# Optimization experiments

Hardware: AMD Instinct MI355X
Metric: run time of the kernel (lower is better)

Reference implementation:

```python
import jax, jax.numpy as jnp
import numpy as np

BATCH = 4096
IN_CAPS = 64
OUT_CAPS = 16
IN_DIM = 64
OUT_DIM = 64
NUM_ITER = 3
LN_EPS = 1e-5


def setup_inputs() -> dict:
    key = jax.random.key(0)
    ks = jax.random.split(key, 13)
    n = lambda k, s: jax.random.normal(k, s, dtype=jnp.float32)
    return {
        "x_inp": n(ks[0], (BATCH, IN_CAPS, IN_DIM)),
        "W_A": n(ks[1], (IN_CAPS, IN_DIM)),
        "B_A": n(ks[2], (IN_CAPS,)),
        "W_F1": n(ks[3], (IN_CAPS, IN_DIM, IN_DIM)),
        "W_F2": n(ks[4], (OUT_CAPS, IN_DIM, OUT_DIM)),
        "B_F2": n(ks[5], (OUT_CAPS, OUT_DIM)),
        "W_G1": n(ks[6], (OUT_DIM, OUT_DIM)),
        "W_G2": n(ks[7], (OUT_CAPS, OUT_DIM, IN_DIM)),
        "B_G2": n(ks[8], (OUT_CAPS, IN_DIM)),
        "ln_gamma": jnp.ones((OUT_DIM,), jnp.float32),
        "ln_beta": jnp.zeros((OUT_DIM,), jnp.float32),
        "W_S": n(ks[9], (IN_CAPS, OUT_CAPS, IN_DIM)),
        "B_S": n(ks[10], (IN_CAPS, OUT_CAPS)),
        "beta_use": n(ks[11], (IN_CAPS, OUT_CAPS)),
        "beta_ign": n(ks[12], (IN_CAPS, OUT_CAPS)),
    }


def _layer_norm(x, gamma, beta):
    mu = jnp.mean(x, axis=-1, keepdims=True)
    var = jnp.var(x, axis=-1, keepdims=True)  # biased, matches torch LayerNorm
    return (x - mu) * jax.lax.rsqrt(var + LN_EPS) * gamma + beta


def reference(x_inp, W_A, B_A, W_F1, W_F2, B_F2, W_G1, W_G2, B_G2,
              ln_gamma, ln_beta, W_S, B_S, beta_use, beta_ign):
    B = x_inp.shape[0]
    inv_sqrt = np.float32(1.0 / np.sqrt(IN_DIM))
    # activation logits per input capsule: [B, in_caps]
    a_e = jnp.einsum('bif,if->bi', x_inp, W_A) * inv_sqrt + B_A
    f_a_e = jax.nn.sigmoid(a_e)  # loop-invariant
    # temp_F is loop-invariant: [B, in_caps, in_dim]
    temp_F = jnp.einsum('bif,ifh->bih', x_inp, W_F1) * inv_sqrt
    R_em = jnp.full((B, IN_CAPS, OUT_CAPS), 1.0 / OUT_CAPS, dtype=x_inp.dtype)
    x_out = None
    for _ in range(NUM_ITER):
        D_use = f_a_e[:, :, None] * R_em                      # [B,i,m]
        D_ign = f_a_e[:, :, None] - D_use                     # [B,i,m]
        phi_em = beta_use * D_use - beta_ign * D_ign          # [B,i,m]
        temp_F_routed = phi_em.sum(axis=-1)[:, :, None] * temp_F  # [B,i,h]
        x_out = jnp.einsum('bih,mhd->bmd', temp_F_routed, W_F2) + B_F2  # [B,m,d]
        x_out_norm = _layer_norm(x_out, ln_gamma, ln_beta)
        temp_G = jnp.einsum('bmd,dh->bmh', x_out_norm, W_G1)  # [B,m,d]
        x_inp_hat = jnp.einsum('bmh,mhi->bmi', temp_G, W_G2) + B_G2  # [B,m,f]
        consistency = jnp.einsum('bif,bmf,imf->bim', x_inp, x_inp_hat, W_S) + B_S
        R_em = jax.nn.softmax(consistency, axis=-1)  # exp(log_softmax)
    return x_out
```

## Files before the change

### kernel.cpp

```cpp
#include <hip/hip_runtime.h>
#include <math.h>

#define IC 64
#define OC 16
#define DIM 64

typedef __attribute__((ext_vector_type(8))) short bf16x8;
typedef __attribute__((ext_vector_type(4))) float f32x4;

__device__ __forceinline__ unsigned short f2bf(float f) {
    unsigned int b = __float_as_uint(f);
    b += 0x7fffu + ((b >> 16) & 1u);
    return (unsigned short)(b >> 16);
}
__device__ __forceinline__ float bf2f(unsigned short h) {
    return __uint_as_float(((unsigned int)h) << 16);
}

__global__ void kSetup(const float* __restrict__ W_F2, const float* __restrict__ W_S,
                       const float* __restrict__ B_S, const float* __restrict__ bu,
                       const float* __restrict__ bi_, const float* __restrict__ W_G1,
                       const float* __restrict__ W_G2,
                       float* __restrict__ WSt2,
                       unsigned short* __restrict__ W1h, unsigned short* __restrict__ W1l,
                       unsigned short* __restrict__ W2h, unsigned short* __restrict__ W2l,
                       float* __restrict__ BSt, float* __restrict__ cb,
                       float* __restrict__ db, float* __restrict__ eb)
{
    int e = blockIdx.x * 256 + threadIdx.x;
    {
        int h = e >> 10, m = (e >> 6) & 15, d = e & 63;
        float v = W_F2[((size_t)m * 64 + h) * 64 + d];
        unsigned short hh = f2bf(v);
        size_t o = ((size_t)m * 64 + d) * 64 + h;
        W1h[o] = hh; W1l[o] = f2bf(v - bf2f(hh));
    }
    {
        int m = e >> 12, fo = (e >> 8) & 15, i = (e >> 2) & 63, fi = e & 3;
        WSt2[e] = W_S[((size_t)i * 16 + m) * 64 + fo * 4 + fi];
    }
    {
        int m = e >> 12, d = (e >> 6) & 63, f = e & 63;
        const float* g1 = W_G1 + d * 64;
        const float* g2 = W_G2 + (size_t)m * 4096 + f;
        float a = 0.f;
#pragma unroll 8
        for (int h = 0; h < 64; h++) a += g1[h] * g2[h * 64];
        unsigned short hh = f2bf(a);
        size_t o = ((size_t)m * 64 + f) * 64 + d;
        W2h[o] = hh; W2l[o] = f2bf(a - bf2f(hh));
    }
    if (e < 1024) {
        int m = e >> 6, i = e & 63;
        BSt[e] = B_S[i * 16 + m];
        cb[e] = bu[e] + bi_[e];
    }
    if (e < 64) {
        float sc = 0.f, sd = 0.f;
        for (int m = 0; m < 16; m++) {
            sc += bu[e * 16 + m] + bi_[e * 16 + m];
            sd += bi_[e * 16 + m];
        }
        db[e] = sd;
        eb[e] = sc * (1.0f / 16.0f) - sd;
    }
}

__global__ __launch_bounds__(256, 4)
void kT(const float* __restrict__ x, const float* __restrict__ W_A,
        const float* __restrict__ B_A, const float* __restrict__ eb,
        float* __restrict__ xq, float* __restrict__ fa, float* __restrict__ phi)
{
    __shared__ float Xs[2 * 64 * 65];
    const int t = threadIdx.x;
    const int blk = blockIdx.x;

    const float4* x4 = (const float4*)x;
#pragma unroll
    for (int s = 0; s < 8; s++) {
        int p = s * 256 + t;
        float4 v = x4[(size_t)blk * 2048 + p];
        int b = p >> 10, i = (p >> 4) & 63, fo = p & 15;
        float* row = &Xs[(b * 64 + i) * 65 + fo * 4];
        row[0] = v.x; row[1] = v.y; row[2] = v.z; row[3] = v.w;
    }
    __syncthreads();

    const int lane = t & 63, w = t >> 6;
#pragma unroll
    for (int s = 0; s < 8; s++) {
        int idx = s * 4 + w;
        int b = idx >> 4, fo = idx & 15;
        const float* row = &Xs[(b * 64 + lane) * 65 + fo * 4];
        ((float4*)xq)[((size_t)(blk * 2 + b) * 16 + fo) * 64 + lane] =
            make_float4(row[0], row[1], row[2], row[3]);
    }

    {
        int p = t >> 1, h = t & 1;
        int b = p >> 6, i = p & 63;
        const float* row = &Xs[(b * 64 + i) * 65 + h * 32];
        const float* wa = W_A + i * 64 + h * 32;
        float v = 0.f;
#pragma unroll
        for (int j = 0; j < 32; j++) v += row[j] * wa[j];
        v += __shfl_xor(v, 1);
        if (h == 0) {
            float ae = v * 0.125f + B_A[i];
            float fv = 1.0f / (1.0f + expf(-ae));
            size_t o = (size_t)(blk * 2 + b) * 64 + i;
            fa[o] = fv;
            phi[o] = fv * eb[i];
        }
    }
}

__global__ __launch_bounds__(256, 4)
void kA(const float* __restrict__ x, const float* __restrict__ W_F1,
        float* __restrict__ tF)
{
    __shared__ unsigned short Ah[64][72], Al[64][72];
    __shared__ unsigned short Bh[64][72], Bl[64][72];
    const int i = blockIdx.y;
    const int b0 = blockIdx.x * 64;
    const int t = threadIdx.x;
    const int bl = t >> 2, q = t & 3;

    {
        const float* src = x + ((size_t)(b0 + bl) * IC + i) * DIM + q * 4;
#pragma unroll
        for (int j4 = 0; j4 < 4; j4++) {
            float4 v = *(const float4*)(src + j4 * 16);
            int f = q * 4 + j4 * 16;
            float vv[4] = {v.x, v.y, v.z, v.w};
            ushort4 h4, l4;
            unsigned short hh;
            hh = f2bf(vv[0]); h4.x = hh; l4.x = f2bf(vv[0] - bf2f(hh));
            hh = f2bf(vv[1]); h4.y = hh; l4.y = f2bf(vv[1] - bf2f(hh));
            hh = f2bf(vv[2]); h4.z = hh; l4.z = f2bf(vv[2] - bf2f(hh));
            hh = f2bf(vv[3]); h4.w = hh; l4.w = f2bf(vv[3] - bf2f(hh));
            *(ushort4*)&Ah[bl][f] = h4;
            *(ushort4*)&Al[bl][f] = l4;
        }
        const float* wsrc = W_F1 + ((size_t)i * DIM + bl) * DIM + q * 4;
#pragma unroll
        for (int j4 = 0; j4 < 4; j4++) {
            float4 v = *(const float4*)(wsrc + j4 * 16);
            int h0 = q * 4 + j4 * 16;
            float vv[4] = {v.x, v.y, v.z, v.w};
#pragma unroll
            for (int c = 0; c < 4; c++) {
                unsigned short hh = f2bf(vv[c]);
                Bh[h0 + c][bl] = hh;
                Bl[h0 + c][bl] = f2bf(vv[c] - bf2f(hh));
            }
        }
    }
    __syncthreads();

    const int w = t >> 6, lane = t & 63;
    const int fm = lane & 15, fq = lane >> 4;
    const int r0 = w * 16;
    f32x4 acc[4];
#pragma unroll
    for (int nt = 0; nt < 4; nt++) {
        acc[nt][0] = 0.f; acc[nt][1] = 0.f; acc[nt][2] = 0.f; acc[nt][3] = 0.f;
    }

#pragma unroll
    for (int ks = 0; ks < 2; ks++) {
        const int kk = ks * 32 + fq * 8;
        bf16x8 ah = *(const bf16x8*)&Ah[r0 + fm][kk];
        bf16x8 al = *(const bf16x8*)&Al[r0 + fm][kk];
#pragma unroll
        for (int nt = 0; nt < 4; nt++) {
            bf16x8 bh = *(const bf16x8*)&Bh[nt * 16 + fm][kk];
            bf16x8 bl2 = *(const bf16x8*)&Bl[nt * 16 + fm][kk];
            acc[nt] = __builtin_amdgcn_mfma_f32_16x16x32_bf16(ah, bh, acc[nt], 0, 0, 0);
            acc[nt] = __builtin_amdgcn_mfma_f32_16x16x32_bf16(ah, bl2, acc[nt], 0, 0, 0);
            acc[nt] = __builtin_amdgcn_mfma_f32_16x16x32_bf16(al, bh, acc[nt], 0, 0, 0);
        }
    }

#pragma unroll
    for (int nt = 0; nt < 4; nt++)
#pragma unroll
        for (int j = 0; j < 4; j++) {
            int row = r0 + fq * 4 + j;
            int col = nt * 16 + fm;
            tF[((size_t)(b0 + row) * IC + i) * DIM + col] = acc[nt][j] * 0.125f;
        }
}

__global__ __launch_bounds__(256, 4)
void kS(const float* __restrict__ phi, const float* __restrict__ tF,
        float* __restrict__ s)
{
    __shared__ float ph[4 * 64];
    const int t = threadIdx.x;
    const int b0 = blockIdx.x * 4;
    ph[t] = phi[(size_t)b0 * 64 + t];
    __syncthreads();

    const int w = t >> 6, lane = t & 63;
    const int ig = lane >> 4, hq = lane & 15;
    const int b = b0 + w;
    const float4* tf4 = (const float4*)(tF + ((size_t)b * 64 + ig * 16) * 64) + hq;
    float4 a = make_float4(0.f, 0.f, 0.f, 0.f);
#pragma unroll
    for (int k = 0; k < 16; k++) {
        float p = ph[w * 64 + ig * 16 + k];
        float4 v = tf4[k * 16];
        a.x += p * v.x; a.y += p * v.y; a.z += p * v.z; a.w += p * v.w;
    }
#pragma unroll
    for (int k = 16; k <= 32; k <<= 1) {
        a.x += __shfl_xor(a.x, k); a.y += __shfl_xor(a.y, k);
        a.z += __shfl_xor(a.z, k); a.w += __shfl_xor(a.w, k);
    }
    if (ig == 0)
        ((float4*)(s + (size_t)b * 64))[hq] = a;
}

__global__ __launch_bounds__(256, 4)
void kXG(const float* __restrict__ s,
         const unsigned short* __restrict__ W1h, const unsigned short* __restrict__ W1l,
         const float* __restrict__ B_F2,
         const unsigned short* __restrict__ W2h, const unsigned short* __restrict__ W2l,
         const float* __restrict__ B_G2,
         const float* __restrict__ gam, const float* __restrict__ bet,
         float* __restrict__ xhat, float* __restrict__ out, const int last)
{
    __shared__ unsigned short Ah[64][72], Al[64][72];
    __shared__ unsigned short Bh[64][72], Bl[64][72];
    const int b0 = blockIdx.x * 64;
    const int m = blockIdx.y;
    const int t = threadIdx.x;
    const int bl = t >> 2, q = t & 3;

    {
        const float* src = s + (size_t)(b0 + bl) * DIM + q * 16;
#pragma unroll
        for (int j4 = 0; j4 < 4; j4++) {
            float4 v = ((const float4*)src)[j4];
            int f = q * 16 + j4 * 4;
            float vv[4] = {v.x, v.y, v.z, v.w};
            ushort4 h4, l4;
            unsigned short hh;
            hh = f2bf(vv[0]); h4.x = hh; l4.x = f2bf(vv[0] - bf2f(hh));
            hh = f2bf(vv[1]); h4.y = hh; l4.y = f2bf(vv[1] - bf2f(hh));
            hh = f2bf(vv[2]); h4.z = hh; l4.z = f2bf(vv[2] - bf2f(hh));
            hh = f2bf(vv[3]); h4.w = hh; l4.w = f2bf(vv[3] - bf2f(hh));
            *(ushort4*)&Ah[bl][f] = h4;
            *(ushort4*)&Al[bl][f] = l4;
        }
        const size_t wo = ((size_t)m * 64 + bl) * 64 + q * 16;
#pragma unroll
        for (int part = 0; part < 2; part++) {
            *(uint4*)&Bh[bl][q * 16 + part * 8] = *(const uint4*)(W1h + wo + part * 8);
            *(uint4*)&Bl[bl][q * 16 + part * 8] = *(const uint4*)(W1l + wo + part * 8);
        }
    }
    __syncthreads();

    const int w = t >> 6, lane = t & 63;
    const int fm = lane & 15, fq = lane >> 4;
    const int r0 = w * 16;
    f32x4 acc[4];
#pragma unroll
    for (int nt = 0; nt < 4; nt++) {
        acc[nt][0] = 0.f; acc[nt][1] = 0.f; acc[nt][2] = 0.f; acc[nt][3] = 0.f;
    }
#pragma unroll
    for (int ks = 0; ks < 2; ks++) {
        const int kk = ks * 32 + fq * 8;
        bf16x8 ah = *(const bf16x8*)&Ah[r0 + fm][kk];
        bf16x8 al = *(const bf16x8*)&Al[r0 + fm][kk];
#pragma unroll
        for (int nt = 0; nt < 4; nt++) {
            bf16x8 bh = *(const bf16x8*)&Bh[nt * 16 + fm][kk];
            bf16x8 bl2 = *(const bf16x8*)&Bl[nt * 16 + fm][kk];
            acc[nt] = __builtin_amdgcn_mfma_f32_16x16x32_bf16(ah, bh, acc[nt], 0, 0, 0);
            acc[nt] = __builtin_amdgcn_mfma_f32_16x16x32_bf16(ah, bl2, acc[nt], 0, 0, 0);
            acc[nt] = __builtin_amdgcn_mfma_f32_16x16x32_bf16(al, bh, acc[nt], 0, 0, 0);
        }
    }
#pragma unroll
    for (int nt = 0; nt < 4; nt++) {
        float bf = B_F2[m * DIM + nt * 16 + fm];
#pragma unroll
        for (int j = 0; j < 4; j++) acc[nt][j] += bf;
    }

    if (last) {
#pragma unroll
        for (int nt = 0; nt < 4; nt++)
#pragma unroll
            for (int j = 0; j < 4; j++) {
                int row = r0 + fq * 4 + j;
                out[((size_t)(b0 + row) * OC + m) * DIM + nt * 16 + fm] = acc[nt][j];
            }
        return;
    }

    {
        float g4[4], b4[4];
#pragma unroll
        for (int nt = 0; nt < 4; nt++) {
            g4[nt] = gam[nt * 16 + fm];
            b4[nt] = bet[nt * 16 + fm];
        }
#pragma unroll
        for (int j = 0; j < 4; j++) {
            float sum = acc[0][j] + acc[1][j] + acc[2][j] + acc[3][j];
            float sq = acc[0][j] * acc[0][j] + acc[1][j] * acc[1][j] +
                       acc[2][j] * acc[2][j] + acc[3][j] * acc[3][j];
#pragma unroll
            for (int k = 1; k <= 8; k <<= 1) {
                sum += __shfl_xor(sum, k);
                sq  += __shfl_xor(sq, k);
            }
            float mu = sum * (1.0f / 64.0f);
            float var = sq * (1.0f / 64.0f) - mu * mu;
            float rs = 1.0f / sqrtf(var + 1e-5f);
#pragma unroll
            for (int nt = 0; nt < 4; nt++)
                acc[nt][j] = (acc[nt][j] - mu) * rs * g4[nt] + b4[nt];
        }
    }
    __syncthreads();

    {
#pragma unroll
        for (int nt = 0; nt < 4; nt++)
#pragma unroll
            for (int j = 0; j < 4; j++) {
                float v = acc[nt][j];
                unsigned short hh = f2bf(v);
                int row = r0 + fq * 4 + j, col = nt * 16 + fm;
                Ah[row][col] = hh;
                Al[row][col] = f2bf(v - bf2f(hh));
            }
        const size_t wo = ((size_t)m * 64 + bl) * 64 + q * 16;
#pragma unroll
        for (int part = 0; part < 2; part++) {
            *(uint4*)&Bh[bl][q * 16 + part * 8] = *(const uint4*)(W2h + wo + part * 8);
            *(uint4*)&Bl[bl][q * 16 + part * 8] = *(const uint4*)(W2l + wo + part * 8);
        }
    }
    __syncthreads();

    f32x4 xh[4];
#pragma unroll
    for (int nt = 0; nt < 4; nt++) {
        float bg = B_G2[m * DIM + nt * 16 + fm];
        xh[nt][0] = bg; xh[nt][1] = bg; xh[nt][2] = bg; xh[nt][3] = bg;
    }
#pragma unroll
    for (int ks = 0; ks < 2; ks++) {
        const int kk = ks * 32 + fq * 8;
        bf16x8 ah = *(const bf16x8*)&Ah[r0 + fm][kk];
        bf16x8 al = *(const bf16x8*)&Al[r0 + fm][kk];
#pragma unroll
        for (int nt = 0; nt < 4; nt++) {
            bf16x8 bh = *(const bf16x8*)&Bh[nt * 16 + fm][kk];
            bf16x8 bl2 = *(const bf16x8*)&Bl[nt * 16 + fm][kk];
            xh[nt] = __builtin_amdgcn_mfma_f32_16x16x32_bf16(ah, bh, xh[nt], 0, 0, 0);
            xh[nt] = __builtin_amdgcn_mfma_f32_16x16x32_bf16(ah, bl2, xh[nt], 0, 0, 0);
            xh[nt] = __builtin_amdgcn_mfma_f32_16x16x32_bf16(al, bh, xh[nt], 0, 0, 0);
        }
    }
#pragma unroll
    for (int nt = 0; nt < 4; nt++)
#pragma unroll
        for (int j = 0; j < 4; j++) {
            int row = r0 + fq * 4 + j;
            xhat[((size_t)(b0 + row) * OC + m) * DIM + nt * 16 + fm] = xh[nt][j];
        }
}

__global__ __launch_bounds__(256, 4)
void kC(const float* __restrict__ xq, const float* __restrict__ xhat,
        const float* __restrict__ WSt2, const float* __restrict__ BSt,
        const float* __restrict__ cb, const float* __restrict__ db,
        const float* __restrict__ fa, const float* __restrict__ tF,
        float* __restrict__ s)
{
    __shared__ float buf[4 * 64 * 17];
    __shared__ float phs[4][64];
    const int b0 = blockIdx.x * 4;
    const int t = threadIdx.x;
    const int w = t >> 6, lane = t & 63;

    {
        const float4* src = (const float4*)(xhat + (size_t)b0 * OC * DIM);
        float4* dst = (float4*)buf;
#pragma unroll
        for (int j = 0; j < 4; j++) dst[t + j * 256] = src[t + j * 256];
    }
    __syncthreads();

    float acc[4][4];
#pragma unroll
    for (int k = 0; k < 4; k++) {
        float bs = BSt[(w * 4 + k) * IC + lane];
#pragma unroll
        for (int g = 0; g < 4; g++) acc[g][k] = bs;
    }

    const float4* xq4 = (const float4*)xq;
    for (int fc = 0; fc < 64; fc += 8) {
        const int fo = fc >> 2;
        float wreg[4][8];
#pragma unroll
        for (int k = 0; k < 4; k++) {
            int m = w * 4 + k;
#pragma unroll
            for (int q2 = 0; q2 < 2; q2++) {
                float4 v = *(const float4*)&WSt2[(((size_t)m * 16 + fo + q2) * IC + lane) * 4];
                wreg[k][q2 * 4 + 0] = v.x; wreg[k][q2 * 4 + 1] = v.y;
                wreg[k][q2 * 4 + 2] = v.z; wreg[k][q2 * 4 + 3] = v.w;
            }
        }
#pragma unroll
        for (int g = 0; g < 4; g++) {
            float xr[8];
#pragma unroll
            for (int q2 = 0; q2 < 2; q2++) {
                float4 v = xq4[((size_t)(b0 + g) * 16 + fo + q2) * 64 + lane];
                xr[q2 * 4 + 0] = v.x; xr[q2 * 4 + 1] = v.y;
                xr[q2 * 4 + 2] = v.z; xr[q2 * 4 + 3] = v.w;
            }
#pragma unroll
            for (int k = 0; k < 4; k++) {
                int m = w * 4 + k;
                const float* hp = &buf[(g * OC + m) * DIM + fc];
                float hr[8];
#pragma unroll
                for (int q2 = 0; q2 < 2; q2++) {
                    float4 v = *(const float4*)(hp + q2 * 4);
                    hr[q2 * 4 + 0] = v.x; hr[q2 * 4 + 1] = v.y;
                    hr[q2 * 4 + 2] = v.z; hr[q2 * 4 + 3] = v.w;
                }
#pragma unroll
                for (int ff = 0; ff < 8; ff++)
                    acc[g][k] += xr[ff] * hr[ff] * wreg[k][ff];
            }
        }
    }
    __syncthreads();
#pragma unroll
    for (int g = 0; g < 4; g++)
#pragma unroll
        for (int k = 0; k < 4; k++)
            buf[(g * IC + lane) * 17 + w * 4 + k] = acc[g][k];
    __syncthreads();

    {
        int g = t >> 6, i = t & 63;
        const float* row = &buf[(g * IC + i) * 17];
        float v[16], mx = -1e30f;
#pragma unroll
        for (int m = 0; m < OC; m++) { v[m] = row[m]; mx = fmaxf(mx, v[m]); }
        float sum = 0.f;
#pragma unroll
        for (int m = 0; m < OC; m++) { v[m] = expf(v[m] - mx); sum += v[m]; }
        float inv = 1.0f / sum;
        float a2 = 0.f;
#pragma unroll
        for (int m = 0; m < OC; m++) a2 += v[m] * inv * cb[i * OC + m];
        phs[g][i] = fa[(size_t)(b0 + g) * IC + i] * (a2 - db[i]);
    }
    __syncthreads();

    {
        const int ig = lane >> 4, hq = lane & 15;
        const int b = b0 + w;
        const float4* tf4 = (const float4*)(tF + ((size_t)b * 64 + ig * 16) * 64) + hq;
        float4 a = make_float4(0.f, 0.f, 0.f, 0.f);
#pragma unroll
        for (int k = 0; k < 16; k++) {
            float p = phs[w][ig * 16 + k];
            float4 v = tf4[k * 16];
            a.x += p * v.x; a.y += p * v.y; a.z += p * v.z; a.w += p * v.w;
        }
#pragma unroll
        for (int k = 16; k <= 32; k <<= 1) {
            a.x += __shfl_xor(a.x, k); a.y += __shfl_xor(a.y, k);
            a.z += __shfl_xor(a.z, k); a.w += __shfl_xor(a.w, k);
        }
        if (ig == 0)
            ((float4*)(s + (size_t)b * 64))[hq] = a;
    }
}

extern "C" void kernel_launch(void* const* d_in, const int* in_sizes, int n_in,
                              void* d_out, int out_size, void* d_ws, size_t ws_size,
                              hipStream_t stream)
{
    const float* x    = (const float*)d_in[0];
    const float* W_A  = (const float*)d_in[1];
    const float* B_A  = (const float*)d_in[2];
    const float* W_F1 = (const float*)d_in[3];
    const float* W_F2 = (const float*)d_in[4];
    const float* B_F2 = (const float*)d_in[5];
    const float* W_G1 = (const float*)d_in[6];
    const float* W_G2 = (const float*)d_in[7];
    const float* B_G2 = (const float*)d_in[8];
    const float* gam  = (const float*)d_in[9];
    const float* bet  = (const float*)d_in[10];
    const float* W_S  = (const float*)d_in[11];
    const float* B_S  = (const float*)d_in[12];
    const float* bu   = (const float*)d_in[13];
    const float* bi_  = (const float*)d_in[14];

    float* ws   = (float*)d_ws;
    float* tF   = ws;
    float* xq   = tF + 16777216;
    float* fa   = xq + 16777216;
    float* phi  = fa + 262144;
    float* s    = phi + 262144;
    float* xhat = s + 262144;
    float* WSt2 = xhat + 4194304;
    unsigned short* W1h = (unsigned short*)(WSt2 + 65536);
    unsigned short* W1l = W1h + 65536;
    unsigned short* W2h = W1l + 65536;
    unsigned short* W2l = W2h + 65536;
    float* BSt  = (float*)(W2l + 65536);
    float* cb   = BSt + 1024;
    float* db   = cb + 1024;
    float* eb   = db + 64;
    float* out  = (float*)d_out;

    kSetup<<<256, 256, 0, stream>>>(W_F2, W_S, B_S, bu, bi_, W_G1, W_G2,
                                    WSt2, W1h, W1l, W2h, W2l, BSt, cb, db, eb);
    kT<<<2048, 256, 0, stream>>>(x, W_A, B_A, eb, xq, fa, phi);
    kA<<<dim3(64, 64), 256, 0, stream>>>(x, W_F1, tF);
    kS<<<1024, 256, 0, stream>>>(phi, tF, s);
    for (int it = 0; it < 3; ++it) {
        kXG<<<dim3(64, 16), 256, 0, stream>>>(s, W1h, W1l, B_F2, W2h, W2l, B_G2,
                                              gam, bet, xhat, out, it == 2 ? 1 : 0);
        if (it < 2)
            kC<<<1024, 256, 0, stream>>>(xq, xhat, WSt2, BSt, cb, db, fa, tF, s);
    }
}
```

Measured before the change: 285.5 us.

## Double batch per kC block and read xhat through uniform scalar loads

kC now handles 8 batch rows per 512-thread block, not 4 per 256-thread block. Each wave pair splits across batch halves while sharing the same W_S slice. The shared-memory staging of xhat and its barrier are removed. Each wave instead reads xhat with wave-uniform addresses marked via readfirstlane, so the loads can go through the scalar path. This is meant to cut LDS traffic and a sync point, but it relies on scalar-cache bandwidth and larger blocks, which may lower occupancy.

Measured after the change: 312.1 us. 1.09x slower.

```diff
diff --git a/kernel.cpp b/kernel.cpp
--- a/kernel.cpp
+++ b/kernel.cpp
@@ -379,42 +379,35 @@
         }
 }
 
-__global__ __launch_bounds__(256, 4)
+__global__ __launch_bounds__(512, 4)
 void kC(const float* __restrict__ xq, const float* __restrict__ xhat,
         const float* __restrict__ WSt2, const float* __restrict__ BSt,
         const float* __restrict__ cb, const float* __restrict__ db,
         const float* __restrict__ fa, const float* __restrict__ tF,
         float* __restrict__ s)
 {
-    __shared__ float buf[4 * 64 * 17];
-    __shared__ float phs[4][64];
-    const int b0 = blockIdx.x * 4;
+    __shared__ float buf[8 * 64 * 17];
+    __shared__ float phs[8][64];
+    const int b0 = blockIdx.x * 8;
     const int t = threadIdx.x;
     const int w = t >> 6, lane = t & 63;
-
-    {
-        const float4* src = (const float4*)(xhat + (size_t)b0 * OC * DIM);
-        float4* dst = (float4*)buf;
-#pragma unroll
-        for (int j = 0; j < 4; j++) dst[t + j * 256] = src[t + j * 256];
-    }
-    __syncthreads();
+    const int mq = w & 3, gh = w >> 2;
 
     float acc[4][4];
 #pragma unroll
     for (int k = 0; k < 4; k++) {
-        float bs = BSt[(w * 4 + k) * IC + lane];
-#pragma unroll
-        for (int g = 0; g < 4; g++) acc[g][k] = bs;
+        float bs = BSt[(mq * 4 + k) * IC + lane];
+#pragma unroll
+        for (int gg = 0; gg < 4; gg++) acc[gg][k] = bs;
     }
 
     const float4* xq4 = (const float4*)xq;
-    for (int fc = 0; fc < 64; fc += 8) {
-        const int fo = fc >> 2;
+    for (int fo8 = 0; fo8 < 8; fo8++) {
+        const int fo = fo8 * 2, fc = fo8 * 8;
         float wreg[4][8];
 #pragma unroll
         for (int k = 0; k < 4; k++) {
-            int m = w * 4 + k;
+            int m = mq * 4 + k;
 #pragma unroll
             for (int q2 = 0; q2 < 2; q2++) {
                 float4 v = *(const float4*)&WSt2[(((size_t)m * 16 + fo + q2) * IC + lane) * 4];
@@ -423,7 +416,8 @@
             }
         }
 #pragma unroll
-        for (int g = 0; g < 4; g++) {
+        for (int gg = 0; gg < 4; gg++) {
+            int g = gh * 4 + gg;
             float xr[8];
 #pragma unroll
             for (int q2 = 0; q2 < 2; q2++) {
@@ -433,27 +427,23 @@
             }
 #pragma unroll
             for (int k = 0; k < 4; k++) {
-                int m = w * 4 + k;
-                const float* hp = &buf[(g * OC + m) * DIM + fc];
-                float hr[8];
-#pragma unroll
-                for (int q2 = 0; q2 < 2; q2++) {
-                    float4 v = *(const float4*)(hp + q2 * 4);
-                    hr[q2 * 4 + 0] = v.x; hr[q2 * 4 + 1] = v.y;
-                    hr[q2 * 4 + 2] = v.z; hr[q2 * 4 + 3] = v.w;
-                }
+                int m = mq * 4 + k;
+                int uo = __builtin_amdgcn_readfirstlane(
+                    (int)(((b0 + g) * 16 + m) * 64 + fc));
+                float4 h0 = *(const float4*)(xhat + uo);
+                float4 h1 = *(const float4*)(xhat + uo + 4);
+                float hs[8] = {h0.x, h0.y, h0.z, h0.w, h1.x, h1.y, h1.z, h1.w};
 #pragma unroll
                 for (int ff = 0; ff < 8; ff++)
-                    acc[g][k] += xr[ff] * hr[ff] * wreg[k][ff];
-            }
-        }
-    }
-    __syncthreads();
-#pragma unroll
-    for (int g = 0; g < 4; g++)
+                    acc[gg][k] += (xr[ff] * wreg[k][ff]) * hs[ff];
+            }
+        }
+    }
+#pragma unroll
+    for (int gg = 0; gg < 4; gg++)
 #pragma unroll
         for (int k = 0; k < 4; k++)
-            buf[(g * IC + lane) * 17 + w * 4 + k] = acc[g][k];
+            buf[((gh * 4 + gg) * IC + lane) * 17 + mq * 4 + k] = acc[gg][k];
     __syncthreads();
 
     {
@@ -541,6 +531,6 @@
         kXG<<<dim3(64, 16), 256, 0, stream>>>(s, W1h, W1l, B_F2, W2h, W2l, B_G2,
                                               gam, bet, xhat, out, it == 2 ? 1 : 0);
         if (it < 2)
-            kC<<<1024, 256, 0, stream>>>(xq, xhat, WSt2, BSt, cb, db, fa, tF, s);
-    }
-}
+            kC<<<512, 512, 0, stream>>>(xq, xhat, WSt2, BSt, cb, db, fa, tF, s);
+    }
+}
```

## Merge setup and transpose kernels; precompute split-bf16 transposed W_F1

Applied to the files above, without the earlier changes.

The weight-setup kernel and the x-transpose/activation kernel are merged into one launch, with the first 256 blocks doing setup and the rest doing the transpose. The eb term is now recomputed per input capsule inside the transpose path, so that path no longer depends on setup output. W_F1 is converted once into transposed bf16 hi/lo arrays, and kA loads these with vector copies instead of converting and scattering W_F1 in every one of its 4096 blocks. This removes one launch and the redundant per-block conversion, at the cost of extra workspace and a small redundant loop over the beta parameters.

New measurement: 279.3 us. 2.2% less time.

```diff
diff --git a/kernel.cpp b/kernel.cpp
--- a/kernel.cpp
+++ b/kernel.cpp
@@ -17,63 +17,71 @@
     return __uint_as_float(((unsigned int)h) << 16);
 }
 
-__global__ void kSetup(const float* __restrict__ W_F2, const float* __restrict__ W_S,
-                       const float* __restrict__ B_S, const float* __restrict__ bu,
-                       const float* __restrict__ bi_, const float* __restrict__ W_G1,
-                       const float* __restrict__ W_G2,
-                       float* __restrict__ WSt2,
-                       unsigned short* __restrict__ W1h, unsigned short* __restrict__ W1l,
-                       unsigned short* __restrict__ W2h, unsigned short* __restrict__ W2l,
-                       float* __restrict__ BSt, float* __restrict__ cb,
-                       float* __restrict__ db, float* __restrict__ eb)
+__global__ __launch_bounds__(256, 4)
+void kF1(const float* __restrict__ W_F2, const float* __restrict__ W_S,
+         const float* __restrict__ B_S, const float* __restrict__ bu,
+         const float* __restrict__ bi_, const float* __restrict__ W_G1,
+         const float* __restrict__ W_G2, const float* __restrict__ W_F1,
+         const float* __restrict__ x, const float* __restrict__ W_A,
+         const float* __restrict__ B_A,
+         float* __restrict__ WSt2,
+         unsigned short* __restrict__ W1h, unsigned short* __restrict__ W1l,
+         unsigned short* __restrict__ W2h, unsigned short* __restrict__ W2l,
+         unsigned short* __restrict__ WF1Th, unsigned short* __restrict__ WF1Tl,
+         float* __restrict__ BSt, float* __restrict__ cb, float* __restrict__ db,
+         float* __restrict__ xq, float* __restrict__ fa, float* __restrict__ phi)
 {
-    int e = blockIdx.x * 256 + threadIdx.x;
-    {
-        int h = e >> 10, m = (e >> 6) & 15, d = e & 63;
-        float v = W_F2[((size_t)m * 64 + h) * 64 + d];
-        unsigned short hh = f2bf(v);
-        size_t o = ((size_t)m * 64 + d) * 64 + h;
-        W1h[o] = hh; W1l[o] = f2bf(v - bf2f(hh));
-    }
-    {
-        int m = e >> 12, fo = (e >> 8) & 15, i = (e >> 2) & 63, fi = e & 3;
-        WSt2[e] = W_S[((size_t)i * 16 + m) * 64 + fo * 4 + fi];
-    }
-    {
-        int m = e >> 12, d = (e >> 6) & 63, f = e & 63;
-        const float* g1 = W_G1 + d * 64;
-        const float* g2 = W_G2 + (size_t)m * 4096 + f;
-        float a = 0.f;
+    if (blockIdx.x < 256) {
+        int e = blockIdx.x * 256 + threadIdx.x;
+        {
+            int h = e >> 10, m = (e >> 6) & 15, d = e & 63;
+            float v = W_F2[((size_t)m * 64 + h) * 64 + d];
+            unsigned short hh = f2bf(v);
+            size_t o = ((size_t)m * 64 + d) * 64 + h;
+            W1h[o] = hh; W1l[o] = f2bf(v - bf2f(hh));
+        }
+        {
+            int m = e >> 12, fo = (e >> 8) & 15, i = (e >> 2) & 63, fi = e & 3;
+            WSt2[e] = W_S[((size_t)i * 16 + m) * 64 + fo * 4 + fi];
+        }
+        {
+            int m = e >> 12, d = (e >> 6) & 63, f = e & 63;
+            const float* g1 = W_G1 + d * 64;
+            const float* g2 = W_G2 + (size_t)m * 4096 + f;
+            float a = 0.f;
 #pragma unroll 8
-        for (int h = 0; h < 64; h++) a += g1[h] * g2[h * 64];
-        unsigned short hh = f2bf(a);
-        size_t o = ((size_t)m * 64 + f) * 64 + d;
-        W2h[o] = hh; W2l[o] = f2bf(a - bf2f(hh));
-    }
-    if (e < 1024) {
-        int m = e >> 6, i = e & 63;
-        BSt[e] = B_S[i * 16 + m];
-        cb[e] = bu[e] + bi_[e];
-    }
-    if (e < 64) {
-        float sc = 0.f, sd = 0.f;
-        for (int m = 0; m < 16; m++) {
-            sc += bu[e * 16 + m] + bi_[e * 16 + m];
-            sd += bi_[e * 16 + m];
-        }
-        db[e] = sd;
-        eb[e] = sc * (1.0f / 16.0f) - sd;
-    }
-}
-
-__global__ __launch_bounds__(256, 4)
-void kT(const float* __restrict__ x, const float* __restrict__ W_A,
-        const float* __restrict__ B_A, const float* __restrict__ eb,
-        float* __restrict__ xq, float* __restrict__ fa, float* __restrict__ phi)
-{
+            for (int h = 0; h < 64; h++) a += g1[h] * g2[h * 64];
+            unsigned short hh = f2bf(a);
+            size_t o = ((size_t)m * 64 + f) * 64 + d;
+            W2h[o] = hh; W2l[o] = f2bf(a - bf2f(hh));
+        }
+        {
+#pragma unroll
+            for (int r = 0; r < 4; r++) {
+                int idx = r * 65536 + e;
+                int i = idx >> 12, h = (idx >> 6) & 63, f = idx & 63;
+                float v = W_F1[(((size_t)i * 64 + f) * 64) + h];
+                unsigned short hh = f2bf(v);
+                size_t o = ((size_t)i * 64 + h) * 64 + f;
+                WF1Th[o] = hh; WF1Tl[o] = f2bf(v - bf2f(hh));
+            }
+        }
+        if (e < 1024) {
+            int m = e >> 6, i = e & 63;
+            BSt[e] = B_S[i * 16 + m];
+            cb[e] = bu[e] + bi_[e];
+        }
+        if (e < 64) {
+            float sd = 0.f;
+            for (int m = 0; m < 16; m++) sd += bi_[e * 16 + m];
+            db[e] = sd;
+        }
+        return;
+    }
+
     __shared__ float Xs[2 * 64 * 65];
     const int t = threadIdx.x;
-    const int blk = blockIdx.x;
+    const int blk = blockIdx.x - 256;
 
     const float4* x4 = (const float4*)x;
 #pragma unroll
@@ -106,17 +114,24 @@
         for (int j = 0; j < 32; j++) v += row[j] * wa[j];
         v += __shfl_xor(v, 1);
         if (h == 0) {
+            float sc = 0.f, sd = 0.f;
+            for (int m = 0; m < 16; m++) {
+                float vu = bu[i * 16 + m], vi = bi_[i * 16 + m];
+                sc += vu + vi; sd += vi;
+            }
+            float ebi = sc * (1.0f / 16.0f) - sd;
             float ae = v * 0.125f + B_A[i];
             float fv = 1.0f / (1.0f + expf(-ae));
             size_t o = (size_t)(blk * 2 + b) * 64 + i;
             fa[o] = fv;
-            phi[o] = fv * eb[i];
+            phi[o] = fv * ebi;
         }
     }
 }
 
 __global__ __launch_bounds__(256, 4)
-void kA(const float* __restrict__ x, const float* __restrict__ W_F1,
+void kA(const float* __restrict__ x,
+        const unsigned short* __restrict__ WF1Th, const unsigned short* __restrict__ WF1Tl,
         float* __restrict__ tF)
 {
     __shared__ unsigned short Ah[64][72], Al[64][72];
@@ -142,18 +157,11 @@
             *(ushort4*)&Ah[bl][f] = h4;
             *(ushort4*)&Al[bl][f] = l4;
         }
-        const float* wsrc = W_F1 + ((size_t)i * DIM + bl) * DIM + q * 4;
-#pragma unroll
-        for (int j4 = 0; j4 < 4; j4++) {
-            float4 v = *(const float4*)(wsrc + j4 * 16);
-            int h0 = q * 4 + j4 * 16;
-            float vv[4] = {v.x, v.y, v.z, v.w};
-#pragma unroll
-            for (int c = 0; c < 4; c++) {
-                unsigned short hh = f2bf(vv[c]);
-                Bh[h0 + c][bl] = hh;
-                Bl[h0 + c][bl] = f2bf(vv[c] - bf2f(hh));
-            }
+        const size_t wo = ((size_t)i * 64 + bl) * 64 + q * 16;
+#pragma unroll
+        for (int part = 0; part < 2; part++) {
+            *(uint4*)&Bh[bl][q * 16 + part * 8] = *(const uint4*)(WF1Th + wo + part * 8);
+            *(uint4*)&Bl[bl][q * 16 + part * 8] = *(const uint4*)(WF1Tl + wo + part * 8);
         }
     }
     __syncthreads();
@@ -529,13 +537,15 @@
     float* BSt  = (float*)(W2l + 65536);
     float* cb   = BSt + 1024;
     float* db   = cb + 1024;
-    float* eb   = db + 64;
+    unsigned short* WF1Th = (unsigned short*)(db + 64);
+    unsigned short* WF1Tl = WF1Th + 262144;
     float* out  = (float*)d_out;
 
-    kSetup<<<256, 256, 0, stream>>>(W_F2, W_S, B_S, bu, bi_, W_G1, W_G2,
-                                    WSt2, W1h, W1l, W2h, W2l, BSt, cb, db, eb);
-    kT<<<2048, 256, 0, stream>>>(x, W_A, B_A, eb, xq, fa, phi);
-    kA<<<dim3(64, 64), 256, 0, stream>>>(x, W_F1, tF);
+    kF1<<<2304, 256, 0, stream>>>(W_F2, W_S, B_S, bu, bi_, W_G1, W_G2, W_F1,
+                                  x, W_A, B_A,
+                                  WSt2, W1h, W1l, W2h, W2l, WF1Th, WF1Tl,
+                                  BSt, cb, db, xq, fa, phi);
+    kA<<<dim3(64, 64), 256, 0, stream>>>(x, WF1Th, WF1Tl, tF);
     kS<<<1024, 256, 0, stream>>>(phi, tF, s);
     for (int it = 0; it < 3; ++it) {
         kXG<<<dim3(64, 16), 256, 0, stream>>>(s, W1h, W1l, B_F2, W2h, W2l, B_G2,
```
